# Kernel tuning notes

Measured on AMD Instinct MI355X. Metric: run time of the kernel, lower is better.

## Reference

```python
import jax, jax.numpy as jnp
import numpy as np

N_NODES = 50000
N_EDGES = 400000


def _gcn_norm(edge_index, num_nodes):
    """Add self-loops and compute symmetric GCN normalization coefficients.

    Returns (src, dst, norm) where out[dst] += norm * h[src].
    """
    loop = jnp.arange(num_nodes, dtype=edge_index.dtype)
    src = jnp.concatenate([edge_index[0], loop])
    dst = jnp.concatenate([edge_index[1], loop])
    ones = jnp.ones(src.shape[0], dtype=jnp.float32)
    deg = jax.ops.segment_sum(ones, dst, num_segments=num_nodes)
    d_inv_sqrt = jnp.where(deg > 0, jax.lax.rsqrt(jnp.maximum(deg, 1.0)), 0.0)
    norm = d_inv_sqrt[src] * d_inv_sqrt[dst]
    return src, dst, norm


def _gcn_conv(x, W, b, src, dst, norm, num_nodes):
    h = x @ W                              # [N, out] dense GEMM first (PyG GCNConv order)
    msg = h[src] * norm[:, None]           # [E+N, out] gather + scale
    agg = jax.ops.segment_sum(msg, dst, num_segments=num_nodes)  # scatter-add
    return agg + b


def setup_inputs() -> dict:
    key = jax.random.key(0)
    k1, k2, k3, k4, k5, k6 = jax.random.split(key, 6)
    x = jax.random.normal(k1, (N_NODES, 128), dtype=jnp.float32)
    edge_index = jax.random.randint(k2, (2, N_EDGES), 0, N_NODES, dtype=jnp.int64)
    # Glorot-ish scaled params
    W1 = jax.random.normal(k3, (128, 512), dtype=jnp.float32) * (1.0 / np.sqrt(128))
    b1 = jnp.zeros((512,), dtype=jnp.float32)
    W2 = jax.random.normal(k4, (512, 250), dtype=jnp.float32) * (1.0 / np.sqrt(512))
    b2 = jnp.zeros((250,), dtype=jnp.float32)
    return {"x": x, "edge_index": edge_index, "W1": W1, "b1": b1, "W2": W2, "b2": b2}


def reference(x, edge_index, W1, b1, W2, b2):
    num_nodes = x.shape[0]
    src, dst, norm = _gcn_norm(edge_index, num_nodes)
    h = _gcn_conv(x, W1, b1, src, dst, norm, num_nodes)
    h = jax.nn.relu(h)
    h = _gcn_conv(h, W2, b2, src, dst, norm, num_nodes)
    return jax.nn.relu(h)
```

## Files before the change

### kernel.cpp

```cpp
#include <hip/hip_runtime.h>

constexpr int NN  = 50000;
constexpr int NE  = 400000;
constexpr int F0  = 128;
constexpr int F1  = 512;
constexpr int F2  = 250;
constexpr int MT64 = 782;
constexpr int SCAN_N = 50176;
constexpr int SCAN_B = 49;

typedef short  short8 __attribute__((ext_vector_type(8)));
typedef float  f32x4  __attribute__((ext_vector_type(4)));

__device__ inline unsigned short f2bf(float f) {
    union { float f; unsigned u; } v; v.f = f;
    unsigned u = v.u;
    return (unsigned short)((u + 0x7FFFu + ((u >> 16) & 1u)) >> 16);
}
__device__ inline float bf2f(unsigned short h) {
    union { unsigned u; float f; } v; v.u = ((unsigned)h) << 16;
    return v.f;
}

__global__ void k_hist(const int4* __restrict__ dst4, int* __restrict__ cnt) {
    int t = blockIdx.x * 256 + threadIdx.x;
    if (t >= NE / 4) return;
    int4 d = dst4[t];
    atomicAdd(&cnt[d.x], 1); atomicAdd(&cnt[d.y], 1);
    atomicAdd(&cnt[d.z], 1); atomicAdd(&cnt[d.w], 1);
}

__global__ __launch_bounds__(256) void k_scanA(const int4* __restrict__ cnt4,
                                               int* __restrict__ bsum) {
    __shared__ int lds[256];
    const int b = blockIdx.x, t = threadIdx.x;
    int4 c = cnt4[b * 256 + t];
    lds[t] = c.x + c.y + c.z + c.w;
    __syncthreads();
    for (int d = 128; d > 0; d >>= 1) {
        if (t < d) lds[t] += lds[t + d];
        __syncthreads();
    }
    if (t == 0) bsum[b] = lds[0];
}
__global__ void k_scanB(const int* __restrict__ bsum, int* __restrict__ boff) {
    int t = threadIdx.x;
    int v = (t < SCAN_B) ? bsum[t] : 0;
    int orig = v;
    for (int d = 1; d < 64; d <<= 1) {
        int u = __shfl_up(v, d);
        if (t >= d) v += u;
    }
    if (t < SCAN_B) boff[t] = v - orig;
}
__global__ __launch_bounds__(256) void k_scanC(const int4* __restrict__ cnt4,
                                               const int* __restrict__ boff,
                                               int* __restrict__ off,
                                               float* __restrict__ dinv) {
    __shared__ int lds[256];
    const int b = blockIdx.x, t = threadIdx.x;
    int4 c = cnt4[b * 256 + t];
    int s = c.x + c.y + c.z + c.w;
    lds[t] = s;
    __syncthreads();
    for (int d = 1; d < 256; d <<= 1) {
        int add = (t >= d) ? lds[t - d] : 0;
        __syncthreads();
        lds[t] += add;
        __syncthreads();
    }
    int run = boff[b] + lds[t] - s;
    int base = b * 1024 + t * 4;
    if (base < NN) { off[base] = run; dinv[base] = rsqrtf((float)c.x + 1.0f); }
    run += c.x;
    if (base + 1 < NN) { off[base + 1] = run; dinv[base + 1] = rsqrtf((float)c.y + 1.0f); }
    run += c.y;
    if (base + 2 < NN) { off[base + 2] = run; dinv[base + 2] = rsqrtf((float)c.z + 1.0f); }
    run += c.z;
    if (base + 3 < NN) { off[base + 3] = run; dinv[base + 3] = rsqrtf((float)c.w + 1.0f); }
    if (b == 0 && t == 0) off[NN] = NE;
}

__global__ void k_bucket(const int4* __restrict__ src4, const int4* __restrict__ dst4,
                         const int* __restrict__ off, int* __restrict__ cnt,
                         int* __restrict__ csr) {
    int t = blockIdx.x * 256 + threadIdx.x;
    if (t >= NE / 4) return;
    int4 s = src4[t];
    int4 d = dst4[t];
    csr[off[d.x] + atomicSub(&cnt[d.x], 1) - 1] = s.x;
    csr[off[d.y] + atomicSub(&cnt[d.y], 1) - 1] = s.y;
    csr[off[d.z] + atomicSub(&cnt[d.z], 1) - 1] = s.z;
    csr[off[d.w] + atomicSub(&cnt[d.w], 1) - 1] = s.w;
}

__global__ __launch_bounds__(256) void k_prep(
        const float4* __restrict__ x4, const float* __restrict__ dinv,
        ushort4* __restrict__ xs,
        const float* __restrict__ W1, unsigned short* __restrict__ w1t,
        const float* __restrict__ W2, unsigned short* __restrict__ w2t) {
    int b = blockIdx.x;
    if (b < 6250) {
        int t = b * 256 + threadIdx.x;
        float dn = dinv[t >> 5];
        float4 v = x4[t];
        ushort4 o;
        o.x = f2bf(dn * v.x); o.y = f2bf(dn * v.y);
        o.z = f2bf(dn * v.z); o.w = f2bf(dn * v.w);
        xs[t] = o;
    } else if (b < 6250 + 256) {
        int t = (b - 6250) * 256 + threadIdx.x;
        int n = t >> 7, k = t & 127;
        w1t[t] = f2bf(W1[k * F1 + n]);
    } else {
        int t = (b - 6506) * 256 + threadIdx.x;
        int n = t >> 9, k = t & 511;
        w2t[t] = (n < F2) ? f2bf(W2[k * F2 + n]) : (unsigned short)0;
    }
}

__global__ __launch_bounds__(256) void k_gather1(
        const ushort4* __restrict__ xs, const int* __restrict__ off,
        const int* __restrict__ csr, const float* __restrict__ dinv,
        ushort4* __restrict__ agg) {
    int n = blockIdx.x * 8 + (threadIdx.x >> 5);
    int c = threadIdx.x & 31;
    if (n >= NN) return;
    float dn = dinv[n];
    ushort4 a = xs[(size_t)n * 32 + c];
    float sx = bf2f(a.x), sy = bf2f(a.y), sz = bf2f(a.z), sw = bf2f(a.w);
    int j = off[n], e1 = off[n + 1];
    for (; j + 4 <= e1; j += 4) {
        int s0 = csr[j], s1 = csr[j + 1], s2 = csr[j + 2], s3 = csr[j + 3];
        ushort4 v0 = xs[(size_t)s0 * 32 + c];
        ushort4 v1 = xs[(size_t)s1 * 32 + c];
        ushort4 v2 = xs[(size_t)s2 * 32 + c];
        ushort4 v3 = xs[(size_t)s3 * 32 + c];
        sx += bf2f(v0.x) + bf2f(v1.x) + bf2f(v2.x) + bf2f(v3.x);
        sy += bf2f(v0.y) + bf2f(v1.y) + bf2f(v2.y) + bf2f(v3.y);
        sz += bf2f(v0.z) + bf2f(v1.z) + bf2f(v2.z) + bf2f(v3.z);
        sw += bf2f(v0.w) + bf2f(v1.w) + bf2f(v2.w) + bf2f(v3.w);
    }
    for (; j < e1; ++j) {
        int s = csr[j];
        ushort4 v = xs[(size_t)s * 32 + c];
        sx += bf2f(v.x); sy += bf2f(v.y); sz += bf2f(v.z); sw += bf2f(v.w);
    }
    ushort4 o;
    o.x = f2bf(dn * sx); o.y = f2bf(dn * sy); o.z = f2bf(dn * sz); o.w = f2bf(dn * sw);
    agg[(size_t)n * 32 + c] = o;
}

__global__ __launch_bounds__(256) void k_gather2(
        const ushort4* __restrict__ t4, const int* __restrict__ off,
        const int* __restrict__ csr, const float* __restrict__ dinv,
        const float* __restrict__ b2, float* __restrict__ out) {
    int n = blockIdx.x * 4 + (threadIdx.x >> 6);
    int c = threadIdx.x & 63;
    if (n >= NN) return;
    float dn = dinv[n];
    ushort4 a = t4[(size_t)n * 64 + c];
    float sx = bf2f(a.x), sy = bf2f(a.y), sz = bf2f(a.z), sw = bf2f(a.w);
    int j = off[n], e1 = off[n + 1];
    for (; j + 4 <= e1; j += 4) {
        int s0 = csr[j], s1 = csr[j + 1], s2 = csr[j + 2], s3 = csr[j + 3];
        ushort4 v0 = t4[(size_t)s0 * 64 + c];
        ushort4 v1 = t4[(size_t)s1 * 64 + c];
        ushort4 v2 = t4[(size_t)s2 * 64 + c];
        ushort4 v3 = t4[(size_t)s3 * 64 + c];
        sx += bf2f(v0.x) + bf2f(v1.x) + bf2f(v2.x) + bf2f(v3.x);
        sy += bf2f(v0.y) + bf2f(v1.y) + bf2f(v2.y) + bf2f(v3.y);
        sz += bf2f(v0.z) + bf2f(v1.z) + bf2f(v2.z) + bf2f(v3.z);
        sw += bf2f(v0.w) + bf2f(v1.w) + bf2f(v2.w) + bf2f(v3.w);
    }
    for (; j < e1; ++j) {
        int s = csr[j];
        ushort4 v = t4[(size_t)s * 64 + c];
        sx += bf2f(v.x); sy += bf2f(v.y); sz += bf2f(v.z); sw += bf2f(v.w);
    }
    int f = c * 4;
    float* o = out + (size_t)n * F2;
    if (f     < F2) o[f]     = fmaxf(dn * sx + b2[f],     0.f);
    if (f + 1 < F2) o[f + 1] = fmaxf(dn * sy + b2[f + 1], 0.f);
    if (f + 2 < F2) o[f + 2] = fmaxf(dn * sz + b2[f + 2], 0.f);
    if (f + 3 < F2) o[f + 3] = fmaxf(dn * sw + b2[f + 3], 0.f);
}

__global__ __launch_bounds__(256) void k_gemm_bf16(
        const unsigned short* __restrict__ A, int lda,
        const unsigned short* __restrict__ Bt, int ldb,
        unsigned short* __restrict__ C, int ldc,
        const float* __restrict__ bias, int do_relu,
        const float* __restrict__ rowscale,
        int M, int K)
{
    __shared__ unsigned short As[2][64 * 32];
    __shared__ unsigned short Bs[2][128 * 32];

    const int tid = threadIdx.x;
    const int wv = tid >> 6, ln = tid & 63;
    const int m0 = blockIdx.y * 64, n0 = blockIdx.x * 128;
    const int wy = wv >> 1, wx = wv & 1;
    const int lane15 = ln & 15, quad = ln >> 4;

    {
    }
    const int cA = tid, mA_ = cA >> 2, qA = cA & 3;
    const int gqA = qA ^ ((mA_ >> 1) & 3);
    int arow = m0 + mA_; if (arow > M - 1) arow = M - 1;
    const unsigned short* agp = A + (size_t)arow * lda + gqA * 8;
    const int aofs = wv * 512;

    const unsigned short* bgp[2];
    int bofs[2];
#pragma unroll
    for (int i = 0; i < 2; ++i) {
        int c = (i * 4 + wv) * 64 + ln;
        int m = c >> 2, q = c & 3;
        int gq = q ^ ((m >> 1) & 3);
        bgp[i] = Bt + (size_t)(n0 + m) * ldb + gq * 8;
        bofs[i] = (i * 4 + wv) * 512;
    }

    f32x4 acc[2][4];
#pragma unroll
    for (int fy = 0; fy < 2; ++fy)
#pragma unroll
        for (int fx = 0; fx < 4; ++fx)
            acc[fy][fx] = (f32x4)0.0f;

    const int NK = K >> 5;

    __builtin_amdgcn_global_load_lds(
        (const __attribute__((address_space(1))) void*)agp,
        (__attribute__((address_space(3))) void*)(&As[0][0] + aofs), 16, 0, 0);
#pragma unroll
    for (int i = 0; i < 2; ++i)
        __builtin_amdgcn_global_load_lds(
            (const __attribute__((address_space(1))) void*)bgp[i],
            (__attribute__((address_space(3))) void*)(&Bs[0][0] + bofs[i]), 16, 0, 0);

    for (int ks = 0; ks < NK; ++ks) {
        __syncthreads();
        if (ks + 1 < NK) {
            int ko = (ks + 1) << 5;
            int nb = (ks + 1) & 1;
            __builtin_amdgcn_global_load_lds(
                (const __attribute__((address_space(1))) void*)(agp + ko),
                (__attribute__((address_space(3))) void*)(&As[nb][0] + aofs), 16, 0, 0);
#pragma unroll
            for (int i = 0; i < 2; ++i)
                __builtin_amdgcn_global_load_lds(
                    (const __attribute__((address_space(1))) void*)(bgp[i] + ko),
                    (__attribute__((address_space(3))) void*)(&Bs[nb][0] + bofs[i]), 16, 0, 0);
        }
        const int b = ks & 1;
        short8 af[2], bf[4];
#pragma unroll
        for (int f = 0; f < 2; ++f) {
            int mA = wy * 32 + f * 16 + lane15;
            int sA = quad ^ ((mA >> 1) & 3);
            af[f] = *(const short8*)(&As[b][0] + mA * 32 + sA * 8);
        }
#pragma unroll
        for (int f = 0; f < 4; ++f) {
            int nB = wx * 64 + f * 16 + lane15;
            int sB = quad ^ ((nB >> 1) & 3);
            bf[f] = *(const short8*)(&Bs[b][0] + nB * 32 + sB * 8);
        }
#pragma unroll
        for (int fy = 0; fy < 2; ++fy)
#pragma unroll
            for (int fx = 0; fx < 4; ++fx)
                acc[fy][fx] = __builtin_amdgcn_mfma_f32_16x16x32_bf16(
                    af[fy], bf[fx], acc[fy][fx], 0, 0, 0);
    }

#pragma unroll
    for (int fy = 0; fy < 2; ++fy) {
        int rowb = m0 + wy * 32 + fy * 16 + quad * 4;
        float rs[4] = {1.f, 1.f, 1.f, 1.f};
        if (rowscale) {
#pragma unroll
            for (int r = 0; r < 4; ++r) {
                int row = rowb + r; if (row > M - 1) row = M - 1;
                rs[r] = rowscale[row];
            }
        }
#pragma unroll
        for (int fx = 0; fx < 4; ++fx) {
            int col = n0 + wx * 64 + fx * 16 + lane15;
            float bia = bias ? bias[col] : 0.0f;
            f32x4 v = acc[fy][fx];
#pragma unroll
            for (int r = 0; r < 4; ++r) {
                int row = rowb + r;
                if (row < M) {
                    float val = v[r] + bia;
                    if (do_relu) val = fmaxf(val, 0.0f);
                    val *= rs[r];
                    C[(size_t)row * ldc + col] = f2bf(val);
                }
            }
        }
    }
}

extern "C" void kernel_launch(void* const* d_in, const int* in_sizes, int n_in,
                              void* d_out, int out_size, void* d_ws, size_t ws_size,
                              hipStream_t stream) {
    const float* x  = (const float*)d_in[0];
    const int*   ei = (const int*)d_in[1];
    const float* W1 = (const float*)d_in[2];
    const float* b1 = (const float*)d_in[3];
    const float* W2 = (const float*)d_in[4];
    const float* b2 = (const float*)d_in[5];
    float* out = (float*)d_out;

    char* p = (char*)d_ws;
    auto carve = [&](size_t bytes) { char* r = p; p += (bytes + 255) & ~(size_t)255; return r; };
    float*          dinv = (float*)carve(NN * 4);
    int*            cnt  = (int*)carve(SCAN_N * 4);
    int*            off  = (int*)carve((NN + 1) * 4);
    int*            csr  = (int*)carve(NE * 4);
    int*            bsum = (int*)carve(64 * 4);
    int*            boff = (int*)carve(64 * 4);
    unsigned short* xs   = (unsigned short*)carve((size_t)NN * F0 * 2);
    unsigned short* agg1 = (unsigned short*)carve((size_t)NN * F0 * 2);
    unsigned short* h1   = (unsigned short*)carve((size_t)NN * F1 * 2);
    unsigned short* t2s  = (unsigned short*)carve((size_t)NN * 256 * 2);
    unsigned short* w1t  = (unsigned short*)carve((size_t)F1 * F0 * 2);
    unsigned short* w2t  = (unsigned short*)carve((size_t)256 * F1 * 2);

    hipMemsetAsync(cnt, 0, SCAN_N * sizeof(int), stream);
    k_hist <<<(NE / 4 + 255) / 256, 256, 0, stream>>>((const int4*)(ei + NE), cnt);
    k_scanA<<<SCAN_B, 256, 0, stream>>>((const int4*)cnt, bsum);
    k_scanB<<<1, 64, 0, stream>>>(bsum, boff);
    k_scanC<<<SCAN_B, 256, 0, stream>>>((const int4*)cnt, boff, off, dinv);
    k_bucket<<<(NE / 4 + 255) / 256, 256, 0, stream>>>(
        (const int4*)ei, (const int4*)(ei + NE), off, cnt, csr);

    k_prep<<<6250 + 256 + 512, 256, 0, stream>>>(
        (const float4*)x, dinv, (ushort4*)xs, W1, w1t, W2, w2t);

    k_gather1<<<(NN + 7) / 8, 256, 0, stream>>>((const ushort4*)xs, off, csr, dinv,
                                                (ushort4*)agg1);
    k_gemm_bf16<<<dim3(F1 / 128, MT64), 256, 0, stream>>>(
        agg1, F0, w1t, F0, h1, F1, b1, 1, nullptr, NN, F0);

    k_gemm_bf16<<<dim3(256 / 128, MT64), 256, 0, stream>>>(
        h1, F1, w2t, F1, t2s, 256, nullptr, 0, dinv, NN, F1);
    k_gather2<<<(NN + 3) / 4, 256, 0, stream>>>((const ushort4*)t2s, off, csr, dinv,
                                                b2, out);
}
```

Measured before the change: 268.2 us.

## Add single-shot K=128 GEMM1, widen gather1 to 64 lanes, unroll gathers by 8

Adds a dedicated layer-1 GEMM that loads the full K=128 A and B tiles into LDS in one pass with direct global-to-LDS loads and an XOR swizzle. This removes the K-loop double-buffering overhead for the small-K GEMM. It also rewrites gather1 to use 64 lanes per node with 32-bit (two bf16) loads, unrolls both gather kernels to eight neighbours per iteration for more memory-level parallelism, and specialises the generic GEMM epilogue to rowscale only. The trade-off is higher LDS use per block (48 KB) and more registers in the gathers, which may lower occupancy.

```diff
diff --git a/kernel.cpp b/kernel.cpp
--- a/kernel.cpp
+++ b/kernel.cpp
@@ -20,6 +20,12 @@
 __device__ inline float bf2f(unsigned short h) {
     union { unsigned u; float f; } v; v.u = ((unsigned)h) << 16;
     return v.f;
+}
+__device__ inline float bflo(unsigned u) {
+    union { unsigned u; float f; } v; v.u = u << 16; return v.f;
+}
+__device__ inline float bfhi(unsigned u) {
+    union { unsigned u; float f; } v; v.u = u & 0xFFFF0000u; return v.f;
 }
 
 __global__ void k_hist(const int4* __restrict__ dst4, int* __restrict__ cnt) {
@@ -120,35 +126,47 @@
 }
 
 __global__ __launch_bounds__(256) void k_gather1(
-        const ushort4* __restrict__ xs, const int* __restrict__ off,
+        const unsigned int* __restrict__ xs, const int* __restrict__ off,
         const int* __restrict__ csr, const float* __restrict__ dinv,
-        ushort4* __restrict__ agg) {
-    int n = blockIdx.x * 8 + (threadIdx.x >> 5);
-    int c = threadIdx.x & 31;
+        unsigned int* __restrict__ agg) {
+    int n = blockIdx.x * 4 + (threadIdx.x >> 6);
+    int c = threadIdx.x & 63;
     if (n >= NN) return;
     float dn = dinv[n];
-    ushort4 a = xs[(size_t)n * 32 + c];
-    float sx = bf2f(a.x), sy = bf2f(a.y), sz = bf2f(a.z), sw = bf2f(a.w);
+    unsigned a = xs[(size_t)n * 64 + c];
+    float s0 = bflo(a), s1 = bfhi(a);
     int j = off[n], e1 = off[n + 1];
+    for (; j + 8 <= e1; j += 8) {
+        int i0 = csr[j],     i1 = csr[j + 1], i2 = csr[j + 2], i3 = csr[j + 3];
+        int i4 = csr[j + 4], i5 = csr[j + 5], i6 = csr[j + 6], i7 = csr[j + 7];
+        unsigned v0 = xs[(size_t)i0 * 64 + c];
+        unsigned v1 = xs[(size_t)i1 * 64 + c];
+        unsigned v2 = xs[(size_t)i2 * 64 + c];
+        unsigned v3 = xs[(size_t)i3 * 64 + c];
+        unsigned v4 = xs[(size_t)i4 * 64 + c];
+        unsigned v5 = xs[(size_t)i5 * 64 + c];
+        unsigned v6 = xs[(size_t)i6 * 64 + c];
+        unsigned v7 = xs[(size_t)i7 * 64 + c];
+        s0 += bflo(v0) + bflo(v1) + bflo(v2) + bflo(v3)
+            + bflo(v4) + bflo(v5) + bflo(v6) + bflo(v7);
+        s1 += bfhi(v0) + bfhi(v1) + bfhi(v2) + bfhi(v3)
+            + bfhi(v4) + bfhi(v5) + bfhi(v6) + bfhi(v7);
+    }
     for (; j + 4 <= e1; j += 4) {
-        int s0 = csr[j], s1 = csr[j + 1], s2 = csr[j + 2], s3 = csr[j + 3];
-        ushort4 v0 = xs[(size_t)s0 * 32 + c];
-        ushort4 v1 = xs[(size_t)s1 * 32 + c];
-        ushort4 v2 = xs[(size_t)s2 * 32 + c];
-        ushort4 v3 = xs[(size_t)s3 * 32 + c];
-        sx += bf2f(v0.x) + bf2f(v1.x) + bf2f(v2.x) + bf2f(v3.x);
-        sy += bf2f(v0.y) + bf2f(v1.y) + bf2f(v2.y) + bf2f(v3.y);
-        sz += bf2f(v0.z) + bf2f(v1.z) + bf2f(v2.z) + bf2f(v3.z);
-        sw += bf2f(v0.w) + bf2f(v1.w) + bf2f(v2.w) + bf2f(v3.w);
+        int i0 = csr[j], i1 = csr[j + 1], i2 = csr[j + 2], i3 = csr[j + 3];
+        unsigned v0 = xs[(size_t)i0 * 64 + c];
+        unsigned v1 = xs[(size_t)i1 * 64 + c];
+        unsigned v2 = xs[(size_t)i2 * 64 + c];
+        unsigned v3 = xs[(size_t)i3 * 64 + c];
+        s0 += bflo(v0) + bflo(v1) + bflo(v2) + bflo(v3);
+        s1 += bfhi(v0) + bfhi(v1) + bfhi(v2) + bfhi(v3);
     }
     for (; j < e1; ++j) {
-        int s = csr[j];
-        ushort4 v = xs[(size_t)s * 32 + c];
-        sx += bf2f(v.x); sy += bf2f(v.y); sz += bf2f(v.z); sw += bf2f(v.w);
-    }
-    ushort4 o;
-    o.x = f2bf(dn * sx); o.y = f2bf(dn * sy); o.z = f2bf(dn * sz); o.w = f2bf(dn * sw);
-    agg[(size_t)n * 32 + c] = o;
+        unsigned v = xs[(size_t)csr[j] * 64 + c];
+        s0 += bflo(v); s1 += bfhi(v);
+    }
+    agg[(size_t)n * 64 + c] =
+        (unsigned)f2bf(dn * s0) | ((unsigned)f2bf(dn * s1) << 16);
 }
 
 __global__ __launch_bounds__(256) void k_gather2(
@@ -162,20 +180,39 @@
     ushort4 a = t4[(size_t)n * 64 + c];
     float sx = bf2f(a.x), sy = bf2f(a.y), sz = bf2f(a.z), sw = bf2f(a.w);
     int j = off[n], e1 = off[n + 1];
+    for (; j + 8 <= e1; j += 8) {
+        int i0 = csr[j],     i1 = csr[j + 1], i2 = csr[j + 2], i3 = csr[j + 3];
+        int i4 = csr[j + 4], i5 = csr[j + 5], i6 = csr[j + 6], i7 = csr[j + 7];
+        ushort4 v0 = t4[(size_t)i0 * 64 + c];
+        ushort4 v1 = t4[(size_t)i1 * 64 + c];
+        ushort4 v2 = t4[(size_t)i2 * 64 + c];
+        ushort4 v3 = t4[(size_t)i3 * 64 + c];
+        ushort4 v4 = t4[(size_t)i4 * 64 + c];
+        ushort4 v5 = t4[(size_t)i5 * 64 + c];
+        ushort4 v6 = t4[(size_t)i6 * 64 + c];
+        ushort4 v7 = t4[(size_t)i7 * 64 + c];
+        sx += bf2f(v0.x) + bf2f(v1.x) + bf2f(v2.x) + bf2f(v3.x)
+            + bf2f(v4.x) + bf2f(v5.x) + bf2f(v6.x) + bf2f(v7.x);
+        sy += bf2f(v0.y) + bf2f(v1.y) + bf2f(v2.y) + bf2f(v3.y)
+            + bf2f(v4.y) + bf2f(v5.y) + bf2f(v6.y) + bf2f(v7.y);
+        sz += bf2f(v0.z) + bf2f(v1.z) + bf2f(v2.z) + bf2f(v3.z)
+            + bf2f(v4.z) + bf2f(v5.z) + bf2f(v6.z) + bf2f(v7.z);
+        sw += bf2f(v0.w) + bf2f(v1.w) + bf2f(v2.w) + bf2f(v3.w)
+            + bf2f(v4.w) + bf2f(v5.w) + bf2f(v6.w) + bf2f(v7.w);
+    }
     for (; j + 4 <= e1; j += 4) {
-        int s0 = csr[j], s1 = csr[j + 1], s2 = csr[j + 2], s3 = csr[j + 3];
-        ushort4 v0 = t4[(size_t)s0 * 64 + c];
-        ushort4 v1 = t4[(size_t)s1 * 64 + c];
-        ushort4 v2 = t4[(size_t)s2 * 64 + c];
-        ushort4 v3 = t4[(size_t)s3 * 64 + c];
+        int i0 = csr[j], i1 = csr[j + 1], i2 = csr[j + 2], i3 = csr[j + 3];
+        ushort4 v0 = t4[(size_t)i0 * 64 + c];
+        ushort4 v1 = t4[(size_t)i1 * 64 + c];
+        ushort4 v2 = t4[(size_t)i2 * 64 + c];
+        ushort4 v3 = t4[(size_t)i3 * 64 + c];
         sx += bf2f(v0.x) + bf2f(v1.x) + bf2f(v2.x) + bf2f(v3.x);
         sy += bf2f(v0.y) + bf2f(v1.y) + bf2f(v2.y) + bf2f(v3.y);
         sz += bf2f(v0.z) + bf2f(v1.z) + bf2f(v2.z) + bf2f(v3.z);
         sw += bf2f(v0.w) + bf2f(v1.w) + bf2f(v2.w) + bf2f(v3.w);
     }
     for (; j < e1; ++j) {
-        int s = csr[j];
-        ushort4 v = t4[(size_t)s * 64 + c];
+        ushort4 v = t4[(size_t)csr[j] * 64 + c];
         sx += bf2f(v.x); sy += bf2f(v.y); sz += bf2f(v.z); sw += bf2f(v.w);
     }
     int f = c * 4;
@@ -186,11 +223,95 @@
     if (f + 3 < F2) o[f + 3] = fmaxf(dn * sw + b2[f + 3], 0.f);
 }
 
+__global__ __launch_bounds__(256) void k_gemm1(
+        const unsigned short* __restrict__ A,
+        const unsigned short* __restrict__ Bt,
+        unsigned short* __restrict__ C,
+        const float* __restrict__ bias, int M)
+{
+    __shared__ unsigned short As[64 * 128];
+    __shared__ unsigned short Bs[128 * 128];
+
+    const int tid = threadIdx.x;
+    const int wv = tid >> 6, ln = tid & 63;
+    const int m0 = blockIdx.y * 64, n0 = blockIdx.x * 128;
+    const int wy = wv >> 1, wx = wv & 1;
+    const int lane15 = ln & 15, quad = ln >> 4;
+
+#pragma unroll
+    for (int i = 0; i < 4; ++i) {
+        int c = i * 256 + tid;
+        int m = c >> 4, q = c & 15;
+        int gq = q ^ (m & 15);
+        int arow = m0 + m; if (arow > M - 1) arow = M - 1;
+        __builtin_amdgcn_global_load_lds(
+            (const __attribute__((address_space(1))) void*)(A + (size_t)arow * 128 + gq * 8),
+            (__attribute__((address_space(3))) void*)(As + (i * 4 + wv) * 512), 16, 0, 0);
+    }
+#pragma unroll
+    for (int i = 0; i < 8; ++i) {
+        int c = i * 256 + tid;
+        int n = c >> 4, q = c & 15;
+        int gq = q ^ (n & 15);
+        __builtin_amdgcn_global_load_lds(
+            (const __attribute__((address_space(1))) void*)(Bt + (size_t)(n0 + n) * 128 + gq * 8),
+            (__attribute__((address_space(3))) void*)(Bs + (i * 4 + wv) * 512), 16, 0, 0);
+    }
+
+    f32x4 acc[2][4];
+#pragma unroll
+    for (int fy = 0; fy < 2; ++fy)
+#pragma unroll
+        for (int fx = 0; fx < 4; ++fx)
+            acc[fy][fx] = (f32x4)0.0f;
+
+    __syncthreads();
+
+#pragma unroll
+    for (int kk = 0; kk < 4; ++kk) {
+        short8 af[2], bf[4];
+#pragma unroll
+        for (int f = 0; f < 2; ++f) {
+            int mA = wy * 32 + f * 16 + lane15;
+            int sA = (kk * 4 + quad) ^ (mA & 15);
+            af[f] = *(const short8*)(As + mA * 128 + sA * 8);
+        }
+#pragma unroll
+        for (int f = 0; f < 4; ++f) {
+            int nB = wx * 64 + f * 16 + lane15;
+            int sB = (kk * 4 + quad) ^ (nB & 15);
+            bf[f] = *(const short8*)(Bs + nB * 128 + sB * 8);
+        }
+#pragma unroll
+        for (int fy = 0; fy < 2; ++fy)
+#pragma unroll
+            for (int fx = 0; fx < 4; ++fx)
+                acc[fy][fx] = __builtin_amdgcn_mfma_f32_16x16x32_bf16(
+                    af[fy], bf[fx], acc[fy][fx], 0, 0, 0);
+    }
+
+#pragma unroll
+    for (int fy = 0; fy < 2; ++fy) {
+        int rowb = m0 + wy * 32 + fy * 16 + quad * 4;
+#pragma unroll
+        for (int fx = 0; fx < 4; ++fx) {
+            int col = n0 + wx * 64 + fx * 16 + lane15;
+            float bia = bias[col];
+            f32x4 v = acc[fy][fx];
+#pragma unroll
+            for (int r = 0; r < 4; ++r) {
+                int row = rowb + r;
+                if (row < M)
+                    C[(size_t)row * F1 + col] = f2bf(fmaxf(v[r] + bia, 0.0f));
+            }
+        }
+    }
+}
+
 __global__ __launch_bounds__(256) void k_gemm_bf16(
         const unsigned short* __restrict__ A, int lda,
         const unsigned short* __restrict__ Bt, int ldb,
         unsigned short* __restrict__ C, int ldc,
-        const float* __restrict__ bias, int do_relu,
         const float* __restrict__ rowscale,
         int M, int K)
 {
@@ -203,8 +324,6 @@
     const int wy = wv >> 1, wx = wv & 1;
     const int lane15 = ln & 15, quad = ln >> 4;
 
-    {
-    }
     const int cA = tid, mA_ = cA >> 2, qA = cA & 3;
     const int gqA = qA ^ ((mA_ >> 1) & 3);
     int arow = m0 + mA_; if (arow > M - 1) arow = M - 1;
@@ -279,28 +398,21 @@
 #pragma unroll
     for (int fy = 0; fy < 2; ++fy) {
         int rowb = m0 + wy * 32 + fy * 16 + quad * 4;
-        float rs[4] = {1.f, 1.f, 1.f, 1.f};
-        if (rowscale) {
-#pragma unroll
-            for (int r = 0; r < 4; ++r) {
-                int row = rowb + r; if (row > M - 1) row = M - 1;
-                rs[r] = rowscale[row];
-            }
+        float rs[4];
+#pragma unroll
+        for (int r = 0; r < 4; ++r) {
+            int row = rowb + r; if (row > M - 1) row = M - 1;
+            rs[r] = rowscale[row];
         }
 #pragma unroll
         for (int fx = 0; fx < 4; ++fx) {
             int col = n0 + wx * 64 + fx * 16 + lane15;
-            float bia = bias ? bias[col] : 0.0f;
             f32x4 v = acc[fy][fx];
 #pragma unroll
             for (int r = 0; r < 4; ++r) {
                 int row = rowb + r;
-                if (row < M) {
-                    float val = v[r] + bia;
-                    if (do_relu) val = fmaxf(val, 0.0f);
-                    val *= rs[r];
-                    C[(size_t)row * ldc + col] = f2bf(val);
-                }
+                if (row < M)
+                    C[(size_t)row * ldc + col] = f2bf(v[r] * rs[r]);
             }
         }
     }
@@ -343,13 +455,12 @@
     k_prep<<<6250 + 256 + 512, 256, 0, stream>>>(
         (const float4*)x, dinv, (ushort4*)xs, W1, w1t, W2, w2t);
 
-    k_gather1<<<(NN + 7) / 8, 256, 0, stream>>>((const ushort4*)xs, off, csr, dinv,
-                                                (ushort4*)agg1);
-    k_gemm_bf16<<<dim3(F1 / 128, MT64), 256, 0, stream>>>(
-        agg1, F0, w1t, F0, h1, F1, b1, 1, nullptr, NN, F0);
+    k_gather1<<<(NN + 3) / 4, 256, 0, stream>>>((const unsigned int*)xs, off, csr,
+                                                dinv, (unsigned int*)agg1);
+    k_gemm1<<<dim3(F1 / 128, MT64), 256, 0, stream>>>(agg1, w1t, h1, b1, NN);
 
     k_gemm_bf16<<<dim3(256 / 128, MT64), 256, 0, stream>>>(
-        h1, F1, w2t, F1, t2s, 256, nullptr, 0, dinv, NN, F1);
+        h1, F1, w2t, F1, t2s, 256, dinv, NN, F1);
     k_gather2<<<(NN + 3) / 4, 256, 0, stream>>>((const ushort4*)t2s, off, csr, dinv,
                                                 b2, out);
 }
```

Measured after the change: 267.3 us. No clear change (-0.3%).
